# Kernel tuning notes

Hardware: AMD Instinct MI355X
Metric: run time of the kernel (lower is better)

Reference implementation:

```python
import jax, jax.numpy as jnp
import numpy as np

H = 64  # hidden size


def _gru_layer(x, w_ih, w_hh, b_ih, b_hh):
    """One GRU layer, torch gate order (r, z, n). x: [B, T, in] -> [B, T, H]."""
    B = x.shape[0]
    # Precompute all input-side gate pre-activations: [B, T, 3H]
    xg = jnp.einsum('bti,gi->btg', x, w_ih) + b_ih
    h0 = jnp.zeros((B, H), x.dtype)

    def step(h, xg_t):  # xg_t: [B, 3H]
        gh = h @ w_hh.T + b_hh  # [B, 3H]
        r = jax.nn.sigmoid(xg_t[:, :H] + gh[:, :H])
        z = jax.nn.sigmoid(xg_t[:, H:2 * H] + gh[:, H:2 * H])
        n = jnp.tanh(xg_t[:, 2 * H:] + r * gh[:, 2 * H:])
        h_new = (1.0 - z) * n + z * h
        return h_new, h_new

    _, ys = jax.lax.scan(step, h0, jnp.swapaxes(xg, 0, 1))  # ys: [T, B, H]
    return jnp.swapaxes(ys, 0, 1)


def setup_inputs() -> dict:
    key = jax.random.key(0)
    ks = jax.random.split(key, 12)
    B, T, I = 512, 1024, 5
    k = 1.0 / np.sqrt(H)  # torch GRU/Linear init range
    u = lambda kk, shape: jax.random.uniform(kk, shape, jnp.float32, -k, k)
    return {
        'x': jax.random.normal(ks[0], (B, T, I), jnp.float32),
        'w_ih0': u(ks[1], (3 * H, I)),
        'w_hh0': u(ks[2], (3 * H, H)),
        'b_ih0': u(ks[3], (3 * H,)),
        'b_hh0': u(ks[4], (3 * H,)),
        'w_ih': u(ks[5], (4, 3 * H, H)),
        'w_hh': u(ks[6], (4, 3 * H, H)),
        'b_ih': u(ks[7], (4, 3 * H)),
        'b_hh': u(ks[8], (4, 3 * H)),
        'w_fc': u(ks[9], (1, H)),
        'b_fc': u(ks[10], (1,)),
    }


def reference(x, w_ih0, w_hh0, b_ih0, b_hh0, w_ih, w_hh, b_ih, b_hh, w_fc, b_fc):
    h = _gru_layer(x, w_ih0, w_hh0, b_ih0, b_hh0)
    for i in range(w_ih.shape[0]):  # layers 1..4 (fixed small count)
        h = _gru_layer(h, w_ih[i], w_hh[i], b_ih[i], b_hh[i])
    # fc on last timestep: [B, H] @ [H, 1] + [1]
    return h[:, -1, :] @ w_fc.T + b_fc
```

## Files before the change

kernel.cpp:

```cpp
#include <hip/hip_runtime.h>
#include <math.h>

#define H 64
#define SEQ_T 1024
#define BATCH 512
#define NTHR 256
#define NBLK BATCH

__device__ __forceinline__ float sigmoid_f(float v) {
    return 1.0f / (1.0f + __expf(-v));
}

__device__ __forceinline__ float tanh_f(float v) {
    float ax = fabsf(v);
    float e = __expf(2.0f * ax);
    float t = 1.0f - 2.0f / (e + 1.0f);
    return copysignf(t, v);
}

#define LDS_BARRIER() asm volatile("s_waitcnt lgkmcnt(0)\n\ts_barrier" ::: "memory")

#define FMA_H(hv, q)                                                            \
    hr = fmaf((hv).x, wHv[0][q].x, hr); hr = fmaf((hv).y, wHv[0][q].y, hr);     \
    hr = fmaf((hv).z, wHv[0][q].z, hr); hr = fmaf((hv).w, wHv[0][q].w, hr);     \
    hz = fmaf((hv).x, wHv[1][q].x, hz); hz = fmaf((hv).y, wHv[1][q].y, hz);     \
    hz = fmaf((hv).z, wHv[1][q].z, hz); hz = fmaf((hv).w, wHv[1][q].w, hz);     \
    hn = fmaf((hv).x, wHv[2][q].x, hn); hn = fmaf((hv).y, wHv[2][q].y, hn);     \
    hn = fmaf((hv).z, wHv[2][q].z, hn); hn = fmaf((hv).w, wHv[2][q].w, hn);

#define FMA_X(xv, q)                                                            \
    ar = fmaf((xv).x, wIv[0][q].x, ar); ar = fmaf((xv).y, wIv[0][q].y, ar);     \
    ar = fmaf((xv).z, wIv[0][q].z, ar); ar = fmaf((xv).w, wIv[0][q].w, ar);     \
    az = fmaf((xv).x, wIv[1][q].x, az); az = fmaf((xv).y, wIv[1][q].y, az);     \
    az = fmaf((xv).z, wIv[1][q].z, az); az = fmaf((xv).w, wIv[1][q].w, az);     \
    an = fmaf((xv).x, wIv[2][q].x, an); an = fmaf((xv).y, wIv[2][q].y, an);     \
    an = fmaf((xv).z, wIv[2][q].z, an); an = fmaf((xv).w, wIv[2][q].w, an);

#define GRU_STEP(X0, X1, X2, X3, PR, PW, TCUR, PPF)                             \
  {                                                                             \
    float4 h0 = *(const float4*)(&hbuf[PR][k0]);                                \
    float4 h1 = *(const float4*)(&hbuf[PR][k0 + 4]);                            \
    float4 h2 = *(const float4*)(&hbuf[PR][k0 + 8]);                            \
    float4 h3 = *(const float4*)(&hbuf[PR][k0 + 12]);                           \
    float ar = 0.f, az = 0.f, an = 0.f, hr = 0.f, hz = 0.f, hn = 0.f;           \
    if (MODE == 0) {                                                            \
                      \
        ar = fmaf(X0.x, wIv[0][0].x, ar); ar = fmaf(X0.y, wIv[0][0].y, ar);     \
        ar = fmaf(X0.z, wIv[0][0].z, ar); ar = fmaf(X0.w, wIv[0][0].w, ar);     \
        ar = fmaf(X1.x, wIv[0][1].x, ar);                                       \
        az = fmaf(X0.x, wIv[1][0].x, az); az = fmaf(X0.y, wIv[1][0].y, az);     \
        az = fmaf(X0.z, wIv[1][0].z, az); az = fmaf(X0.w, wIv[1][0].w, az);     \
        az = fmaf(X1.x, wIv[1][1].x, az);                                       \
        an = fmaf(X0.x, wIv[2][0].x, an); an = fmaf(X0.y, wIv[2][0].y, an);     \
        an = fmaf(X0.z, wIv[2][0].z, an); an = fmaf(X0.w, wIv[2][1].x, an);     \
        an = fmaf(X1.x, wIv[2][1].y, an);                                       \
    } else {                                                                    \
        FMA_X(X0, 0) FMA_X(X1, 1) FMA_X(X2, 2) FMA_X(X3, 3)                     \
    }                                                                           \
    FMA_H(h0, 0) FMA_H(h1, 1) FMA_H(h2, 2) FMA_H(h3, 3)                         \
                         \
    if (MODE == 0) {                                                            \
        if (ks == 0 && (TCUR) + 2 < SEQ_T) {                                    \
            X0 = make_float4(PPF[0], PPF[1], PPF[2], PPF[3]); X1.x = PPF[4];    \
        }                                                                       \
        PPF += 10;                                                              \
    } else {                                                                    \
        if ((TCUR) + 2 < SEQ_T) {                                               \
            const float4* pa_ = (const float4*)PPF;                             \
            X0 = pa_[0]; X1 = pa_[1]; X2 = pa_[2]; X3 = pa_[3];                 \
        }                                                                       \
        PPF += 2 * H;                                                           \
    }                                                                           \
    float sR = ar + hr, sZ = az + hz, sN = an, sH = hn;                         \
    sR += __shfl_xor(sR, 16, 64); sR += __shfl_xor(sR, 32, 64);                 \
    sZ += __shfl_xor(sZ, 16, 64); sZ += __shfl_xor(sZ, 32, 64);                 \
    sN += __shfl_xor(sN, 16, 64); sN += __shfl_xor(sN, 32, 64);                 \
    sH += __shfl_xor(sH, 16, 64); sH += __shfl_xor(sH, 32, 64);                 \
    float r = sigmoid_f(sR + bR);                                               \
    float z = sigmoid_f(sZ + bZ);                                               \
    float n = tanh_f(sN + bNi + r * (sH + bNh));                                \
    float hnew = fmaf(z, hprev - n, n);                      \
    hprev = hnew;                                                               \
    if (ks == 0) {                                                              \
        hbuf[PW][j] = hnew;                                                     \
        if (MODE < 2) *pSt = hnew;                                              \
    }                                                                           \
    pSt += H;                                                                   \
    LDS_BARRIER();                                                              \
  }

template <int MODE>
__device__ __forceinline__ float run_layer(
    const float* __restrict__ xin,
    float* __restrict__ actb,
    float (*hbuf)[H],
    const float4 (&wIv)[3][4], const float4 (&wHv)[3][4],
    float bR, float bZ, float bNi, float bNh,
    int j, int k0, int ks)
{
    float hprev = 0.0f;
    if (ks == 0) hbuf[0][j] = 0.0f;

    float4 xA0, xA1, xA2, xA3, xB0, xB1, xB2, xB3;
    xA0 = xA1 = xA2 = xA3 = make_float4(0.f, 0.f, 0.f, 0.f);
    xB0 = xB1 = xB2 = xB3 = xA0;

    const float* pPFA;
    const float* pPFB;
    if (MODE == 0) {
        if (ks == 0) {
            const float* p0 = xin;
            const float* p1 = xin + 5;
            xA0 = make_float4(p0[0], p0[1], p0[2], p0[3]); xA1.x = p0[4];
            xB0 = make_float4(p1[0], p1[1], p1[2], p1[3]); xB1.x = p1[4];
        }
        pPFA = xin + 10;
        pPFB = xin + 15;
    } else {
        const float4* a0 = (const float4*)(xin + 0 * H + k0);
        const float4* a1 = (const float4*)(xin + 1 * H + k0);
        xA0 = a0[0]; xA1 = a0[1]; xA2 = a0[2]; xA3 = a0[3];
        xB0 = a1[0]; xB1 = a1[1]; xB2 = a1[2]; xB3 = a1[3];
        pPFA = xin + 2 * H + k0;
        pPFB = xin + 3 * H + k0;
    }
    float* pSt = actb + j;

    __syncthreads();

    for (int t = 0; t < SEQ_T; t += 2) {
        GRU_STEP(xA0, xA1, xA2, xA3, 0, 1, t,     pPFA)
        GRU_STEP(xB0, xB1, xB2, xB3, 1, 0, t + 1, pPFB)
    }
    return hprev;
}

__global__ __launch_bounds__(NTHR, 2) void gru_all_kernel(
    const float* __restrict__ x,
    const float* __restrict__ w_ih0, const float* __restrict__ w_hh0,
    const float* __restrict__ b_ih0, const float* __restrict__ b_hh0,
    const float* __restrict__ w_ih, const float* __restrict__ w_hh,
    const float* __restrict__ b_ih, const float* __restrict__ b_hh,
    const float* __restrict__ w_fc, const float* __restrict__ b_fc,
    float* __restrict__ out, float* __restrict__ act)
{
    __shared__ __align__(16) float hbuf[2][H];
    __shared__ float partial[4];

    const int tid  = threadIdx.x;
    const int wv   = tid >> 6;
    const int lane = tid & 63;
    const int jl   = lane & 15;
    const int ks   = lane >> 4;
    const int j    = wv * 16 + jl;
    const int k0   = ks * 16;
    const int b    = blockIdx.x;

    float* __restrict__ actb = act + (size_t)b * (SEQ_T * H);
    const float* __restrict__ xb = x + (size_t)b * (SEQ_T * 5);

    float hlast = 0.0f;
    float4 wIv[3][4], wHv[3][4];

    for (int layer = 0; layer < 5; ++layer) {
        {
            const float* whp = (layer == 0) ? w_hh0 : w_hh + (size_t)(layer - 1) * (192 * H);
            #pragma unroll
            for (int g = 0; g < 3; ++g) {
                const float4* row = (const float4*)(whp + (g * 64 + j) * H + k0);
                #pragma unroll
                for (int q = 0; q < 4; ++q) wHv[g][q] = row[q];
            }
            if (layer == 0) {
                #pragma unroll
                for (int g = 0; g < 3; ++g)
                    #pragma unroll
                    for (int q = 0; q < 4; ++q) wIv[g][q] = make_float4(0.f, 0.f, 0.f, 0.f);
                if (ks == 0) {
                    #pragma unroll
                    for (int g = 0; g < 3; ++g) {
                        const float* row = w_ih0 + (g * 64 + j) * 5;
                        wIv[g][0] = make_float4(row[0], row[1], row[2], row[3]);
                        wIv[g][1].x = row[4];
                    }
                    const float* row2 = w_ih0 + (2 * 64 + j) * 5;
                    wIv[2][0] = make_float4(row2[0], row2[1], row2[2], 0.f);
                    wIv[2][1].x = row2[3];
                    wIv[2][1].y = row2[4];
                }
            } else {
                const float* wip = w_ih + (size_t)(layer - 1) * (192 * H);
                #pragma unroll
                for (int g = 0; g < 3; ++g) {
                    const float4* row = (const float4*)(wip + (g * 64 + j) * H + k0);
                    #pragma unroll
                    for (int q = 0; q < 4; ++q) wIv[g][q] = row[q];
                }
            }
        }

        float bR, bZ, bNi, bNh;
        {
            const float* bip = (layer == 0) ? b_ih0 : b_ih + (layer - 1) * 192;
            const float* bhp = (layer == 0) ? b_hh0 : b_hh + (layer - 1) * 192;
            bR  = bip[j] + bhp[j];
            bZ  = bip[j + 64] + bhp[j + 64];
            bNi = bip[j + 128];
            bNh = bhp[j + 128];
        }

        if (layer == 0)
            hlast = run_layer<0>(xb, actb, hbuf, wIv, wHv, bR, bZ, bNi, bNh, j, k0, ks);
        else if (layer < 4)
            hlast = run_layer<1>(actb, actb, hbuf, wIv, wHv, bR, bZ, bNi, bNh, j, k0, ks);
        else
            hlast = run_layer<2>(actb, actb, hbuf, wIv, wHv, bR, bZ, bNi, bNh, j, k0, ks);
    }

    float v = (ks == 0) ? hlast * w_fc[j] : 0.0f;
    v += __shfl_xor(v, 1, 64);
    v += __shfl_xor(v, 2, 64);
    v += __shfl_xor(v, 4, 64);
    v += __shfl_xor(v, 8, 64);
    if (lane == 0) partial[wv] = v;
    __syncthreads();
    if (tid == 0) out[b] = partial[0] + partial[1] + partial[2] + partial[3] + b_fc[0];
}

extern "C" void kernel_launch(void* const* d_in, const int* in_sizes, int n_in,
                              void* d_out, int out_size, void* d_ws, size_t ws_size,
                              hipStream_t stream) {
    const float* x     = (const float*)d_in[0];
    const float* w_ih0 = (const float*)d_in[1];
    const float* w_hh0 = (const float*)d_in[2];
    const float* b_ih0 = (const float*)d_in[3];
    const float* b_hh0 = (const float*)d_in[4];
    const float* w_ih  = (const float*)d_in[5];
    const float* w_hh  = (const float*)d_in[6];
    const float* b_ih  = (const float*)d_in[7];
    const float* b_hh  = (const float*)d_in[8];
    const float* w_fc  = (const float*)d_in[9];
    const float* b_fc  = (const float*)d_in[10];
    float* out = (float*)d_out;
    float* act = (float*)d_ws;

    hipLaunchKernelGGL(gru_all_kernel, dim3(NBLK), dim3(NTHR), 0, stream,
                       x, w_ih0, w_hh0, b_ih0, b_hh0,
                       w_ih, w_hh, b_ih, b_hh, w_fc, b_fc, out, act);
}
```

Before: 3.557 ms.

## Halve block to 128 threads with 2-way K split per hidden unit

Each batch row's block now uses 2 wavefronts instead of 4, and each hidden unit's dot products are split over 2 lanes with 32 inputs each instead of 4 lanes with 16. Per-thread weight registers double, and the cross-lane reduction drops from two shuffle stages to one. Fewer wavefronts take part in each per-step barrier, which should make synchronisation cheaper. The cost is a longer serial FMA chain per step and much higher register pressure, with launch bounds relaxed to 1 block per CU.

```diff
diff --git a/kernel.cpp b/kernel.cpp
--- a/kernel.cpp
+++ b/kernel.cpp
@@ -4,7 +4,7 @@
 #define H 64
 #define SEQ_T 1024
 #define BATCH 512
-#define NTHR 256
+#define NTHR 128
 #define NBLK BATCH
 
 __device__ __forceinline__ float sigmoid_f(float v) {
@@ -36,29 +36,27 @@
     an = fmaf((xv).x, wIv[2][q].x, an); an = fmaf((xv).y, wIv[2][q].y, an);     \
     an = fmaf((xv).z, wIv[2][q].z, an); an = fmaf((xv).w, wIv[2][q].w, an);
 
-#define GRU_STEP(X0, X1, X2, X3, PR, PW, TCUR, PPF)                             \
+#define GRU_STEP(X0, X1, X2, X3, X4, X5, X6, X7, PR, PW, TCUR, PPF)             \
   {                                                                             \
     float4 h0 = *(const float4*)(&hbuf[PR][k0]);                                \
     float4 h1 = *(const float4*)(&hbuf[PR][k0 + 4]);                            \
     float4 h2 = *(const float4*)(&hbuf[PR][k0 + 8]);                            \
     float4 h3 = *(const float4*)(&hbuf[PR][k0 + 12]);                           \
+    float4 h4 = *(const float4*)(&hbuf[PR][k0 + 16]);                           \
+    float4 h5 = *(const float4*)(&hbuf[PR][k0 + 20]);                           \
+    float4 h6 = *(const float4*)(&hbuf[PR][k0 + 24]);                           \
+    float4 h7 = *(const float4*)(&hbuf[PR][k0 + 28]);                           \
     float ar = 0.f, az = 0.f, an = 0.f, hr = 0.f, hz = 0.f, hn = 0.f;           \
     if (MODE == 0) {                                                            \
-                      \
-        ar = fmaf(X0.x, wIv[0][0].x, ar); ar = fmaf(X0.y, wIv[0][0].y, ar);     \
-        ar = fmaf(X0.z, wIv[0][0].z, ar); ar = fmaf(X0.w, wIv[0][0].w, ar);     \
-        ar = fmaf(X1.x, wIv[0][1].x, ar);                                       \
-        az = fmaf(X0.x, wIv[1][0].x, az); az = fmaf(X0.y, wIv[1][0].y, az);     \
-        az = fmaf(X0.z, wIv[1][0].z, az); az = fmaf(X0.w, wIv[1][0].w, az);     \
-        az = fmaf(X1.x, wIv[1][1].x, az);                                       \
-        an = fmaf(X0.x, wIv[2][0].x, an); an = fmaf(X0.y, wIv[2][0].y, an);     \
-        an = fmaf(X0.z, wIv[2][0].z, an); an = fmaf(X0.w, wIv[2][1].x, an);     \
-        an = fmaf(X1.x, wIv[2][1].y, an);                                       \
+          \
+        FMA_X(X0, 0) FMA_X(X1, 1)                                               \
     } else {                                                                    \
         FMA_X(X0, 0) FMA_X(X1, 1) FMA_X(X2, 2) FMA_X(X3, 3)                     \
+        FMA_X(X4, 4) FMA_X(X5, 5) FMA_X(X6, 6) FMA_X(X7, 7)                     \
     }                                                                           \
     FMA_H(h0, 0) FMA_H(h1, 1) FMA_H(h2, 2) FMA_H(h3, 3)                         \
-                         \
+    FMA_H(h4, 4) FMA_H(h5, 5) FMA_H(h6, 6) FMA_H(h7, 7)                         \
+                   \
     if (MODE == 0) {                                                            \
         if (ks == 0 && (TCUR) + 2 < SEQ_T) {                                    \
             X0 = make_float4(PPF[0], PPF[1], PPF[2], PPF[3]); X1.x = PPF[4];    \
@@ -68,14 +66,16 @@
         if ((TCUR) + 2 < SEQ_T) {                                               \
             const float4* pa_ = (const float4*)PPF;                             \
             X0 = pa_[0]; X1 = pa_[1]; X2 = pa_[2]; X3 = pa_[3];                 \
+            X4 = pa_[4]; X5 = pa_[5]; X6 = pa_[6]; X7 = pa_[7];                 \
         }                                                                       \
         PPF += 2 * H;                                                           \
     }                                                                           \
+                        \
     float sR = ar + hr, sZ = az + hz, sN = an, sH = hn;                         \
-    sR += __shfl_xor(sR, 16, 64); sR += __shfl_xor(sR, 32, 64);                 \
-    sZ += __shfl_xor(sZ, 16, 64); sZ += __shfl_xor(sZ, 32, 64);                 \
-    sN += __shfl_xor(sN, 16, 64); sN += __shfl_xor(sN, 32, 64);                 \
-    sH += __shfl_xor(sH, 16, 64); sH += __shfl_xor(sH, 32, 64);                 \
+    sR += __shfl_xor(sR, 32, 64);                                               \
+    sZ += __shfl_xor(sZ, 32, 64);                                               \
+    sN += __shfl_xor(sN, 32, 64);                                               \
+    sH += __shfl_xor(sH, 32, 64);                                               \
     float r = sigmoid_f(sR + bR);                                               \
     float z = sigmoid_f(sZ + bZ);                                               \
     float n = tanh_f(sN + bNi + r * (sH + bNh));                                \
@@ -94,16 +94,17 @@
     const float* __restrict__ xin,
     float* __restrict__ actb,
     float (*hbuf)[H],
-    const float4 (&wIv)[3][4], const float4 (&wHv)[3][4],
+    const float4 (&wIv)[3][8], const float4 (&wHv)[3][8],
     float bR, float bZ, float bNi, float bNh,
     int j, int k0, int ks)
 {
     float hprev = 0.0f;
     if (ks == 0) hbuf[0][j] = 0.0f;
 
-    float4 xA0, xA1, xA2, xA3, xB0, xB1, xB2, xB3;
-    xA0 = xA1 = xA2 = xA3 = make_float4(0.f, 0.f, 0.f, 0.f);
-    xB0 = xB1 = xB2 = xB3 = xA0;
+    float4 xA0, xA1, xA2, xA3, xA4, xA5, xA6, xA7;
+    float4 xB0, xB1, xB2, xB3, xB4, xB5, xB6, xB7;
+    xA0 = xA1 = xA2 = xA3 = xA4 = xA5 = xA6 = xA7 = make_float4(0.f, 0.f, 0.f, 0.f);
+    xB0 = xB1 = xB2 = xB3 = xB4 = xB5 = xB6 = xB7 = xA0;
 
     const float* pPFA;
     const float* pPFB;
@@ -120,7 +121,9 @@
         const float4* a0 = (const float4*)(xin + 0 * H + k0);
         const float4* a1 = (const float4*)(xin + 1 * H + k0);
         xA0 = a0[0]; xA1 = a0[1]; xA2 = a0[2]; xA3 = a0[3];
+        xA4 = a0[4]; xA5 = a0[5]; xA6 = a0[6]; xA7 = a0[7];
         xB0 = a1[0]; xB1 = a1[1]; xB2 = a1[2]; xB3 = a1[3];
+        xB4 = a1[4]; xB5 = a1[5]; xB6 = a1[6]; xB7 = a1[7];
         pPFA = xin + 2 * H + k0;
         pPFB = xin + 3 * H + k0;
     }
@@ -129,13 +132,13 @@
     __syncthreads();
 
     for (int t = 0; t < SEQ_T; t += 2) {
-        GRU_STEP(xA0, xA1, xA2, xA3, 0, 1, t,     pPFA)
-        GRU_STEP(xB0, xB1, xB2, xB3, 1, 0, t + 1, pPFB)
+        GRU_STEP(xA0, xA1, xA2, xA3, xA4, xA5, xA6, xA7, 0, 1, t,     pPFA)
+        GRU_STEP(xB0, xB1, xB2, xB3, xB4, xB5, xB6, xB7, 1, 0, t + 1, pPFB)
     }
     return hprev;
 }
 
-__global__ __launch_bounds__(NTHR, 2) void gru_all_kernel(
+__global__ __launch_bounds__(NTHR, 1) void gru_all_kernel(
     const float* __restrict__ x,
     const float* __restrict__ w_ih0, const float* __restrict__ w_hh0,
     const float* __restrict__ b_ih0, const float* __restrict__ b_hh0,
@@ -145,22 +148,22 @@
     float* __restrict__ out, float* __restrict__ act)
 {
     __shared__ __align__(16) float hbuf[2][H];
-    __shared__ float partial[4];
+    __shared__ float partial[2];
 
     const int tid  = threadIdx.x;
     const int wv   = tid >> 6;
     const int lane = tid & 63;
-    const int jl   = lane & 15;
-    const int ks   = lane >> 4;
-    const int j    = wv * 16 + jl;
-    const int k0   = ks * 16;
+    const int jl   = lane & 31;
+    const int ks   = lane >> 5;
+    const int j    = wv * 32 + jl;
+    const int k0   = ks * 32;
     const int b    = blockIdx.x;
 
     float* __restrict__ actb = act + (size_t)b * (SEQ_T * H);
     const float* __restrict__ xb = x + (size_t)b * (SEQ_T * 5);
 
     float hlast = 0.0f;
-    float4 wIv[3][4], wHv[3][4];
+    float4 wIv[3][8], wHv[3][8];
 
     for (int layer = 0; layer < 5; ++layer) {
         {
@@ -169,13 +172,13 @@
             for (int g = 0; g < 3; ++g) {
                 const float4* row = (const float4*)(whp + (g * 64 + j) * H + k0);
                 #pragma unroll
-                for (int q = 0; q < 4; ++q) wHv[g][q] = row[q];
+                for (int q = 0; q < 8; ++q) wHv[g][q] = row[q];
             }
             if (layer == 0) {
                 #pragma unroll
                 for (int g = 0; g < 3; ++g)
                     #pragma unroll
-                    for (int q = 0; q < 4; ++q) wIv[g][q] = make_float4(0.f, 0.f, 0.f, 0.f);
+                    for (int q = 0; q < 8; ++q) wIv[g][q] = make_float4(0.f, 0.f, 0.f, 0.f);
                 if (ks == 0) {
                     #pragma unroll
                     for (int g = 0; g < 3; ++g) {
@@ -183,10 +186,6 @@
                         wIv[g][0] = make_float4(row[0], row[1], row[2], row[3]);
                         wIv[g][1].x = row[4];
                     }
-                    const float* row2 = w_ih0 + (2 * 64 + j) * 5;
-                    wIv[2][0] = make_float4(row2[0], row2[1], row2[2], 0.f);
-                    wIv[2][1].x = row2[3];
-                    wIv[2][1].y = row2[4];
                 }
             } else {
                 const float* wip = w_ih + (size_t)(layer - 1) * (192 * H);
@@ -194,7 +193,7 @@
                 for (int g = 0; g < 3; ++g) {
                     const float4* row = (const float4*)(wip + (g * 64 + j) * H + k0);
                     #pragma unroll
-                    for (int q = 0; q < 4; ++q) wIv[g][q] = row[q];
+                    for (int q = 0; q < 8; ++q) wIv[g][q] = row[q];
                 }
             }
         }
@@ -222,9 +221,10 @@
     v += __shfl_xor(v, 2, 64);
     v += __shfl_xor(v, 4, 64);
     v += __shfl_xor(v, 8, 64);
+    v += __shfl_xor(v, 16, 64);
     if (lane == 0) partial[wv] = v;
     __syncthreads();
-    if (tid == 0) out[b] = partial[0] + partial[1] + partial[2] + partial[3] + b_fc[0];
+    if (tid == 0) out[b] = partial[0] + partial[1] + b_fc[0];
 }
 
 extern "C" void kernel_launch(void* const* d_in, const int* in_sizes, int n_in,
```

Measured after the change: 4.378 ms. +23.1%, slower.
